# Kernel tuning notes

Measured on AMD Instinct MI355X. Metric: run time of the kernel, lower is better.

The kernel has to match this reference:

```python
import jax, jax.numpy as jnp
import numpy as np

N, E, G = 4096, 16384, 128   # nodes, edges, graphs
IN, H, ED = 64, 64, 16       # in_dim, hidden, edge_dim


def _lin(key, fan_in, fan_out):
    return jax.random.normal(key, (fan_in, fan_out), dtype=jnp.float32) * (fan_in ** -0.5)


def setup_inputs() -> dict:
    key = jax.random.key(0)
    ks = jax.random.split(key, 32)
    inp = {
        "x": jax.random.normal(ks[0], (N, IN), dtype=jnp.float32),
        "edge_index": jax.random.randint(ks[1], (2, E), 0, N, dtype=jnp.int32),
        "edge_attr": jax.random.normal(ks[2], (E, ED), dtype=jnp.float32),
        "batch": jnp.sort(jax.random.randint(ks[3], (N,), 0, G, dtype=jnp.int32)),
    }
    ki = 4
    dims = [(IN, H), (H, H), (H, H)]  # (in_channels, out_channels) per layer
    for l, (ic, oc) in enumerate(dims):
        hd = ic * oc  # edge-MLP width = hidden * in_channels
        inp[f"l{l}_w1"] = _lin(ks[ki], ED, hd); ki += 1
        inp[f"l{l}_b1"] = jnp.zeros((hd,), dtype=jnp.float32)
        inp[f"l{l}_w2"] = _lin(ks[ki], hd, hd); ki += 1
        inp[f"l{l}_b2"] = jnp.zeros((hd,), dtype=jnp.float32)
        inp[f"l{l}_root"] = _lin(ks[ki], ic, oc); ki += 1
        inp[f"l{l}_bias"] = jnp.zeros((oc,), dtype=jnp.float32)
    return inp


def _nnconv(x, src, dst, edge_attr, w1, b1, w2, b2, root, bias, ic, oc):
    # per-edge weight matrix Theta(e): [E, ic, oc]
    h = jax.nn.relu(edge_attr @ w1 + b1)
    theta = (h @ w2 + b2).reshape(-1, ic, oc)
    # gather source features, per-edge bmm, scatter-mean to target
    msg = jnp.einsum("ei,eio->eo", x[src], theta)
    agg = jax.ops.segment_sum(msg, dst, num_segments=N)
    cnt = jax.ops.segment_sum(jnp.ones((msg.shape[0],), msg.dtype), dst, num_segments=N)
    agg = agg / jnp.maximum(cnt, 1.0)[:, None]
    return agg + x @ root + bias


def reference(x, edge_index, edge_attr, batch,
              l0_w1, l0_b1, l0_w2, l0_b2, l0_root, l0_bias,
              l1_w1, l1_b1, l1_w2, l1_b2, l1_root, l1_bias,
              l2_w1, l2_b1, l2_w2, l2_b2, l2_root, l2_bias):
    src, dst = edge_index[0], edge_index[1]
    layers = [
        (l0_w1, l0_b1, l0_w2, l0_b2, l0_root, l0_bias, IN, H),
        (l1_w1, l1_b1, l1_w2, l1_b2, l1_root, l1_bias, H, H),
        (l2_w1, l2_b1, l2_w2, l2_b2, l2_root, l2_bias, H, H),
    ]
    h = x
    for (w1, b1, w2, b2, root, bias, ic, oc) in layers:
        h = jax.nn.relu(_nnconv(h, src, dst, edge_attr, w1, b1, w2, b2, root, bias, ic, oc))
        # dropout is identity in eval mode
    # global mean pool over graphs
    s = jax.ops.segment_sum(h, batch, num_segments=G)
    c = jax.ops.segment_sum(jnp.ones((N,), h.dtype), batch, num_segments=G)
    return s / jnp.maximum(c, 1.0)[:, None]
```

## Files before the change

### kernel.cpp

```cpp
#include <hip/hip_runtime.h>
#include <hip/hip_bf16.h>

#define NN 4096
#define EE 16384
#define GG 128
#define EDIM 16
#define HD 4096

#define NGROUPS 64
#define GK 8
#define KSUBS 64
#define MAXT 40
#define MAXSLOT (MAXT * 16)
#define MAXTW 5
#define SYUNITS (64 * 65 * 8)
#define PANEL (8 * 64 * 64)

typedef __attribute__((ext_vector_type(8))) short short8;
typedef __attribute__((ext_vector_type(4))) float float4v;

static __device__ inline unsigned short f2b(float f) {
    unsigned u = __float_as_uint(f);
    unsigned r = u + 0x7fff + ((u >> 16) & 1);
    return (unsigned short)(r >> 16);
}

static __device__ inline unsigned pk2(float a, float b) {
    __hip_bfloat162 p = __float22bfloat162_rn(make_float2(a, b));
    return *(unsigned*)&p;
}

__global__ void hker(const float* __restrict__ ea, const float* __restrict__ w1,
                     const float* __restrict__ b1, unsigned short* __restrict__ hB) {
    __shared__ float sea[16 * 16];
    const int tid = threadIdx.x;
    const int j = blockIdx.x * 256 + tid;
    const int e0 = blockIdx.y * 16;
    float w[16];
#pragma unroll
    for (int k = 0; k < 16; ++k) w[k] = w1[k * HD + j];
    const float b = b1[j];
    sea[tid] = ea[e0 * EDIM + tid];
    __syncthreads();
#pragma unroll 4
    for (int el = 0; el < 16; ++el) {
        float a = b;
#pragma unroll
        for (int k = 0; k < 16; ++k) a += sea[el * 16 + k] * w[k];
        hB[(size_t)(e0 + el) * HD + j] = f2b(fmaxf(a, 0.f));
    }
}

__global__ void wperm(const float* __restrict__ w2, unsigned short* __restrict__ W2q) {
    __shared__ float t[64 * 65];
    const int k = blockIdx.x;
    const int tid = threadIdx.x;
    const int o = tid & 63, r4 = tid >> 6;
#pragma unroll
    for (int it = 0; it < 16; ++it) {
        int i = it * 4 + r4;
        t[i * 65 + o] = w2[(size_t)k * HD + i * 64 + o];
    }
    __syncthreads();
    const int o2 = tid >> 2, q = tid & 3;
    const int q2 = q >> 1;
    const int j0 = (o2 >> 4) * 2 + q2;
    const int lmm = o2 & 15;
    const int blk = k;
#pragma unroll
    for (int cc = 0; cc < 2; ++cc) {
        const int quad = (q & 1) * 2 + cc;
        const int ib = q * 16 + cc * 8;
        size_t base = ((size_t)(blk * 64 + quad * 16 + lmm)) * 64 + j0 * 8;
        unsigned b0 = pk2(t[(ib + 0) * 65 + o2], t[(ib + 1) * 65 + o2]);
        unsigned b1 = pk2(t[(ib + 2) * 65 + o2], t[(ib + 3) * 65 + o2]);
        unsigned b2_ = pk2(t[(ib + 4) * 65 + o2], t[(ib + 5) * 65 + o2]);
        unsigned b3 = pk2(t[(ib + 6) * 65 + o2], t[(ib + 7) * 65 + o2]);
        *(uint4*)(&W2q[base]) = make_uint4(b0, b1, b2_, b3);
    }
}

__global__ void count_edges(const int* __restrict__ src, const int* __restrict__ dst,
                            int* __restrict__ cnt_src, float* __restrict__ cnt_dst) {
    const int e = blockIdx.x * 256 + threadIdx.x;
    atomicAdd(&cnt_src[src[e]], 1);
    atomicAdd(&cnt_dst[dst[e]], 1.f);
}

__global__ void build_layout(const int* __restrict__ cnt_src, int* __restrict__ node_slot_base,
                             int* __restrict__ tile_cluster, int* __restrict__ group_ntiles) {
    const int g = threadIdx.x;
    int nt = 0;
    int slot = g * MAXSLOT;
    for (int c = 0; c < 16; ++c) {
        int d = 0;
        for (int j = 0; j < 4; ++j) {
            int n = g * 64 + c * 4 + j;
            node_slot_base[n] = slot + d;
            d += cnt_src[n];
        }
        int tcnt = (d + 15) >> 4;
        if (nt + tcnt > MAXT) tcnt = MAXT - nt;
        for (int j = 0; j < tcnt; ++j) tile_cluster[g * MAXT + nt + j] = c;
        nt += tcnt;
        slot += tcnt * 16;
    }
    group_ntiles[g] = nt;
}

__global__ void fill_slots(const int* __restrict__ src, const int* __restrict__ dst,
                           int* __restrict__ fill, const int* __restrict__ node_slot_base,
                           int* __restrict__ slot_info) {
    const int e = blockIdx.x * 256 + threadIdx.x;
    const int n = src[e];
    const int pos = atomicAdd(&fill[n], 1);
    const int s = node_slot_base[n] + pos;
    const int g = n >> 6;
    if (s < g * MAXSLOT + MAXSLOT)
        slot_info[s] = e | ((n & 3) << 14) | (dst[e] << 16);
}

__global__ void xb_ker(const float* __restrict__ xcur, const float* __restrict__ b2,
                       float* __restrict__ xb) {
    const int n = blockIdx.x * 4 + (threadIdx.x >> 6);
    const int o = threadIdx.x & 63;
    float a = 0.f;
#pragma unroll
    for (int i = 0; i < 64; ++i) a += xcur[n * 64 + i] * b2[i * 64 + o];
    xb[n * 64 + o] = a;
}

__global__ void b2scatter(const float* __restrict__ xb, const int* __restrict__ src,
                          const int* __restrict__ dst, float* __restrict__ agg) {
    const int e = blockIdx.x * 4 + (threadIdx.x >> 6);
    const int o = threadIdx.x & 63;
    atomicAdd(&agg[(size_t)dst[e] * 64 + o], xb[(size_t)src[e] * 64 + o]);
}

__global__ __launch_bounds__(512, 2)
void ygemm_msg(const float* __restrict__ xcur, const unsigned short* __restrict__ hB,
               const unsigned short* __restrict__ W2q, const int* __restrict__ slot_info,
               const int* __restrict__ tile_cluster, const int* __restrict__ group_ntiles,
               float* __restrict__ agg) {
    __shared__ __align__(16) unsigned short sA[64 * 72];
    __shared__ __align__(16) unsigned short sY[2 * SYUNITS];

    const int bid = blockIdx.x;
    const int g = bid >> 3;
    const int kc = bid & 7;
    const int tid = threadIdx.x;
    const int lane = tid & 63, wave = tid >> 6;
    const int quad = lane >> 4, lm = lane & 15;

    {
        const int n = tid >> 3, ib = (tid & 7) * 8;
        const float* xp = xcur + (size_t)(g * 64 + n) * 64 + ib;
        uint4 w = make_uint4(pk2(xp[0], xp[1]), pk2(xp[2], xp[3]),
                             pk2(xp[4], xp[5]), pk2(xp[6], xp[7]));
        *(uint4*)(&sA[n * 72 + ib]) = w;
    }

    const int ntiles = group_ntiles[g];
    int infoR[MAXTW], voff[MAXTW], rbase[MAXTW];
    unsigned shl5[MAXTW];
#pragma unroll
    for (int ai = 0; ai < MAXTW; ++ai) {
        const int ti = wave + ai * 8;
        const int info = (ti < ntiles) ? slot_info[g * MAXSLOT + ti * 16 + lm] : -1;
        const int tc   = (ti < ntiles) ? tile_cluster[g * MAXT + ti] : 0;
        infoR[ai] = info;
        voff[ai]  = ((info >= 0) ? (info & 0x3FFF) : EE) * HD + quad * 2;
        rbase[ai] = ((tc * 4 + quad) * 65 + lm) * 8;
        shl5[ai]  = (unsigned)(((info >> 14) & 3) * 16);
    }

    float4v acc2[MAXTW][4];
#pragma unroll
    for (int a = 0; a < MAXTW; ++a)
#pragma unroll
        for (int t = 0; t < 4; ++t) {
            acc2[a][t][0] = 0.f; acc2[a][t][1] = 0.f;
            acc2[a][t][2] = 0.f; acc2[a][t][3] = 0.f;
        }

    const int qg = wave >> 1, half = wave & 1;
    const int wbase = ((quad * 4 + qg) * 65 + lm) * 8 + half * 4;
    __syncthreads();

    short8 af[4][2];
#pragma unroll
    for (int s = 0; s < 4; ++s)
#pragma unroll
        for (int q2 = 0; q2 < 2; ++q2)
            af[s][q2] = *(const short8*)(&sA[(s * 16 + lm) * 72 + q2 * 32 + quad * 8]);

    const float4v z4 = {0.f, 0.f, 0.f, 0.f};

    const unsigned short* wp  = W2q + ((size_t)(kc * KSUBS * 8 + wave) * 64 + lane) * 64;
    const unsigned short* hbk = hB + kc * KSUBS * 8;

    short8 bfA[4][2], bfB[4][2];
    unsigned hdA[MAXTW], hdB[MAXTW];
#pragma unroll
    for (int tt = 0; tt < 4; ++tt) {
        bfA[tt][0] = *(const short8*)(wp + (tt * 2 + 0) * 8);
        bfA[tt][1] = *(const short8*)(wp + (tt * 2 + 1) * 8);
    }
    wp += PANEL;
#pragma unroll
    for (int ai = 0; ai < MAXTW; ++ai) hdA[ai] = *(const unsigned*)(hbk + voff[ai]);
    hbk += 8;

    auto subody = [&](short8 (&BF)[4][2], unsigned (&HDc)[MAXTW],
                      short8 (&BFN)[4][2], unsigned (&HDN)[MAXTW],
                      unsigned short* __restrict__ sYp) {
#pragma unroll
        for (int s = 0; s < 4; ++s) {
            float4v a1[4];
#pragma unroll
            for (int tt = 0; tt < 4; ++tt)
                a1[tt] = __builtin_amdgcn_mfma_f32_16x16x32_bf16(af[s][0], BF[tt][0], z4, 0, 0, 0);
#pragma unroll
            for (int tt = 0; tt < 4; ++tt)
                a1[tt] = __builtin_amdgcn_mfma_f32_16x16x32_bf16(af[s][1], BF[tt][1], a1[tt], 0, 0, 0);
#pragma unroll
            for (int tt = 0; tt < 4; ++tt) {
                uint2 v;
                v.x = pk2(a1[tt][0], a1[tt][1]);
                v.y = pk2(a1[tt][2], a1[tt][3]);
                *(uint2*)(&sYp[wbase + s * 8320 + tt * 128]) = v;
            }
        }
        __syncthreads();

#pragma unroll
        for (int tt = 0; tt < 4; ++tt) {
            BFN[tt][0] = *(const short8*)(wp + (tt * 2 + 0) * 8);
            BFN[tt][1] = *(const short8*)(wp + (tt * 2 + 1) * 8);
        }
        wp += PANEL;
#pragma unroll
        for (int ai = 0; ai < MAXTW; ++ai)
            HDN[ai] = *(const unsigned*)(hbk + voff[ai]);
        hbk += 8;

#pragma unroll
        for (int ai = 0; ai < MAXTW; ++ai) {
            if (wave + ai * 8 < ntiles) {
                const unsigned h0 = HDc[ai];
                unsigned long long A = (unsigned long long)(h0 & 0xffffu) << shl5[ai];
                unsigned long long B = (unsigned long long)(h0 >> 16) << shl5[ai];
                uint4 aw = make_uint4((unsigned)A, (unsigned)(A >> 32),
                                      (unsigned)B, (unsigned)(B >> 32));
                short8 a2 = *(short8*)&aw;
#pragma unroll
                for (int ot = 0; ot < 4; ++ot) {
                    short8 b2f = *(const short8*)(&sYp[rbase[ai] + ot * 128]);
                    acc2[ai][ot] = __builtin_amdgcn_mfma_f32_16x16x32_bf16(a2, b2f, acc2[ai][ot], 0, 0, 0);
                }
            }
        }
    };

    for (int su2 = 0; su2 < KSUBS; su2 += 2) {
        subody(bfA, hdA, bfB, hdB, sY);
        subody(bfB, hdB, bfA, hdA, sY + SYUNITS);
    }

#pragma unroll
    for (int ai = 0; ai < MAXTW; ++ai) {
        const int ti = wave + ai * 8;
        if (ti < ntiles) {
#pragma unroll
            for (int r = 0; r < 4; ++r) {
                const int inf2 = __shfl(infoR[ai], quad * 4 + r, 64);
                if (inf2 >= 0) {
                    const int d = inf2 >> 16;
#pragma unroll
                    for (int ot = 0; ot < 4; ++ot)
                        atomicAdd(&agg[(size_t)d * 64 + ot * 16 + lm], acc2[ai][ot][r]);
                }
            }
        }
    }
}

__global__ void combine(const float* __restrict__ agg, const float* __restrict__ cnt,
                        const float* __restrict__ xcur, const float* __restrict__ root,
                        const float* __restrict__ bias, float* __restrict__ xn) {
    const int n = blockIdx.x * 4 + (threadIdx.x >> 6);
    const int o = threadIdx.x & 63;
    float a = agg[n * 64 + o] / fmaxf(cnt[n], 1.f);
    float r = bias[o];
#pragma unroll
    for (int i = 0; i < 64; ++i) r += xcur[n * 64 + i] * root[i * 64 + o];
    xn[n * 64 + o] = fmaxf(a + r, 0.f);
}

__global__ void pool_accum(const float* __restrict__ x3, const int* __restrict__ batch,
                           float* __restrict__ pool, float* __restrict__ pcnt) {
    const int n = blockIdx.x * 4 + (threadIdx.x >> 6);
    const int o = threadIdx.x & 63;
    const int gi = batch[n];
    atomicAdd(&pool[gi * 64 + o], x3[n * 64 + o]);
    if (o == 0) atomicAdd(&pcnt[gi], 1.f);
}

__global__ void pool_norm(const float* __restrict__ pool, const float* __restrict__ pcnt,
                          float* __restrict__ out) {
    const int idx = blockIdx.x * 256 + threadIdx.x;
    out[idx] = pool[idx] / fmaxf(pcnt[idx >> 6], 1.f);
}

extern "C" void kernel_launch(void* const* d_in, const int* in_sizes, int n_in,
                              void* d_out, int out_size, void* d_ws, size_t ws_size,
                              hipStream_t stream) {
    const float* x   = (const float*)d_in[0];
    const int*   ei  = (const int*)d_in[1];
    const float* ea  = (const float*)d_in[2];
    const int*   bat = (const int*)d_in[3];
    const int* srcp = ei;
    const int* dstp = ei + EE;

    char* ws = (char*)d_ws;
    size_t off = 0;
    unsigned short* hB  = (unsigned short*)(ws + off); off += (size_t)(EE + 1) * HD * 2;
    unsigned short* W2q = (unsigned short*)(ws + off); off += ((size_t)HD * HD + PANEL) * 2;
    int* slot_info      = (int*)(ws + off); off += (size_t)NGROUPS * MAXSLOT * 4;
    int* tile_cluster   = (int*)(ws + off); off += (size_t)NGROUPS * MAXT * 4;
    int* group_ntiles   = (int*)(ws + off); off += 1024;
    int* node_slot_base = (int*)(ws + off); off += (size_t)NN * 4;
    int* cnt_src        = (int*)(ws + off); off += (size_t)NN * 4;
    int* fillc          = (int*)(ws + off); off += (size_t)NN * 4;
    float* cnt_dst      = (float*)(ws + off); off += (size_t)NN * 4;
    float* agg  = (float*)(ws + off); off += (size_t)NN * 64 * 4;
    float* xb   = (float*)(ws + off); off += (size_t)NN * 64 * 4;
    float* xb0  = (float*)(ws + off); off += (size_t)NN * 64 * 4;
    float* xb1  = (float*)(ws + off); off += (size_t)NN * 64 * 4;
    float* pool = (float*)(ws + off); off += (size_t)GG * 64 * 4;
    float* pcnt = (float*)(ws + off); off += (size_t)GG * 4;

    hipMemsetAsync(slot_info, 0xFF, (size_t)NGROUPS * MAXSLOT * 4, stream);
    hipMemsetAsync(cnt_src, 0, (size_t)NN * 4 * 3, stream);
    hipMemsetAsync(hB + (size_t)EE * HD, 0, (size_t)HD * 2, stream);
    count_edges<<<EE / 256, 256, 0, stream>>>(srcp, dstp, cnt_src, cnt_dst);
    build_layout<<<1, 64, 0, stream>>>(cnt_src, node_slot_base, tile_cluster, group_ntiles);
    fill_slots<<<EE / 256, 256, 0, stream>>>(srcp, dstp, fillc, node_slot_base, slot_info);

    const float* xcur = x;
    float* xbufs[2] = {xb0, xb1};

    for (int l = 0; l < 3; ++l) {
        const float* w1   = (const float*)d_in[4 + 6 * l + 0];
        const float* b1   = (const float*)d_in[4 + 6 * l + 1];
        const float* w2   = (const float*)d_in[4 + 6 * l + 2];
        const float* b2   = (const float*)d_in[4 + 6 * l + 3];
        const float* root = (const float*)d_in[4 + 6 * l + 4];
        const float* bias = (const float*)d_in[4 + 6 * l + 5];

        wperm<<<HD, 256, 0, stream>>>(w2, W2q);
        hker<<<dim3(HD / 256, EE / 16), 256, 0, stream>>>(ea, w1, b1, hB);
        xb_ker<<<NN / 4, 256, 0, stream>>>(xcur, b2, xb);
        hipMemsetAsync(agg, 0, (size_t)NN * 64 * 4, stream);
        b2scatter<<<EE / 4, 256, 0, stream>>>(xb, srcp, dstp, agg);
        ygemm_msg<<<NGROUPS * GK, 512, 0, stream>>>(xcur, hB, W2q, slot_info,
                                                    tile_cluster, group_ntiles, agg);
        float* xn = xbufs[l & 1];
        combine<<<NN / 4, 256, 0, stream>>>(agg, cnt_dst, xcur, root, bias, xn);
        xcur = xn;
    }
    hipMemsetAsync(pool, 0, (size_t)GG * 64 * 4 + (size_t)GG * 4, stream);
    pool_accum<<<NN / 4, 256, 0, stream>>>(xcur, bat, pool, pcnt);
    pool_norm<<<GG * 64 / 256, 256, 0, stream>>>(pool, pcnt, (float*)d_out);
}
```

Baseline: 1.703 ms.

## Halve node groups to 32 nodes and use 256-thread blocks in message GEMM

Node groups shrink from 64 to 32 nodes, which doubles the number of groups and blocks, and each block drops to 4 waves. Each wave now covers its W2 panel in two k-halves per sub-step. The explicit double-buffered B-fragment prefetch is replaced by loading fragments inside the loop, with only the hB values prefetched one step ahead. The aim is more blocks across the CUs and lower per-block LDS and register pressure. The cost is that each W2 panel is now read by twice as many blocks, and the prefetch overlap for weight loads is lost.

Measured after the change: 2.076 ms. +21.9%, slower.

```diff
diff --git a/kernel.cpp b/kernel.cpp
--- a/kernel.cpp
+++ b/kernel.cpp
@@ -7,14 +7,15 @@
 #define EDIM 16
 #define HD 4096
 
-#define NGROUPS 64
+#define NGROUPS 128
 #define GK 8
 #define KSUBS 64
-#define MAXT 40
+#define MAXT 24
 #define MAXSLOT (MAXT * 16)
-#define MAXTW 5
-#define SYUNITS (64 * 65 * 8)
+#define MAXTW 6
+#define SYU 17152
 #define PANEL (8 * 64 * 64)
+#define KHOFF (4 * 64 * 64)
 
 typedef __attribute__((ext_vector_type(8))) short short8;
 typedef __attribute__((ext_vector_type(4))) float float4v;
@@ -92,10 +93,10 @@
     const int g = threadIdx.x;
     int nt = 0;
     int slot = g * MAXSLOT;
-    for (int c = 0; c < 16; ++c) {
+    for (int c = 0; c < 8; ++c) {
         int d = 0;
         for (int j = 0; j < 4; ++j) {
-            int n = g * 64 + c * 4 + j;
+            int n = g * 32 + c * 4 + j;
             node_slot_base[n] = slot + d;
             d += cnt_src[n];
         }
@@ -115,7 +116,7 @@
     const int n = src[e];
     const int pos = atomicAdd(&fill[n], 1);
     const int s = node_slot_base[n] + pos;
-    const int g = n >> 6;
+    const int g = n >> 5;
     if (s < g * MAXSLOT + MAXSLOT)
         slot_info[s] = e | ((n & 3) << 14) | (dst[e] << 16);
 }
@@ -137,13 +138,13 @@
     atomicAdd(&agg[(size_t)dst[e] * 64 + o], xb[(size_t)src[e] * 64 + o]);
 }
 
-__global__ __launch_bounds__(512, 2)
+__global__ __launch_bounds__(256, 2)
 void ygemm_msg(const float* __restrict__ xcur, const unsigned short* __restrict__ hB,
                const unsigned short* __restrict__ W2q, const int* __restrict__ slot_info,
                const int* __restrict__ tile_cluster, const int* __restrict__ group_ntiles,
                float* __restrict__ agg) {
-    __shared__ __align__(16) unsigned short sA[64 * 72];
-    __shared__ __align__(16) unsigned short sY[2 * SYUNITS];
+    __shared__ __align__(16) unsigned short sA[32 * 72];
+    __shared__ __align__(16) unsigned short sY[2 * SYU];
 
     const int bid = blockIdx.x;
     const int g = bid >> 3;
@@ -154,7 +155,7 @@
 
     {
         const int n = tid >> 3, ib = (tid & 7) * 8;
-        const float* xp = xcur + (size_t)(g * 64 + n) * 64 + ib;
+        const float* xp = xcur + (size_t)(g * 32 + n) * 64 + ib;
         uint4 w = make_uint4(pk2(xp[0], xp[1]), pk2(xp[2], xp[3]),
                              pk2(xp[4], xp[5]), pk2(xp[6], xp[7]));
         *(uint4*)(&sA[n * 72 + ib]) = w;
@@ -165,12 +166,12 @@
     unsigned shl5[MAXTW];
 #pragma unroll
     for (int ai = 0; ai < MAXTW; ++ai) {
-        const int ti = wave + ai * 8;
+        const int ti = wave + ai * 4;
         const int info = (ti < ntiles) ? slot_info[g * MAXSLOT + ti * 16 + lm] : -1;
         const int tc   = (ti < ntiles) ? tile_cluster[g * MAXT + ti] : 0;
         infoR[ai] = info;
         voff[ai]  = ((info >= 0) ? (info & 0x3FFF) : EE) * HD + quad * 2;
-        rbase[ai] = ((tc * 4 + quad) * 65 + lm) * 8;
+        rbase[ai] = ((tc * 4 + quad) * 67 + lm) * 8;
         shl5[ai]  = (unsigned)(((info >> 14) & 3) * 16);
     }
 
@@ -184,12 +185,12 @@
         }
 
     const int qg = wave >> 1, half = wave & 1;
-    const int wbase = ((quad * 4 + qg) * 65 + lm) * 8 + half * 4;
+    const int wb0 = ((quad * 4 + qg) * 67 + lm) * 8 + half * 4;
     __syncthreads();
 
-    short8 af[4][2];
-#pragma unroll
-    for (int s = 0; s < 4; ++s)
+    short8 af[2][2];
+#pragma unroll
+    for (int s = 0; s < 2; ++s)
 #pragma unroll
         for (int q2 = 0; q2 < 2; ++q2)
             af[s][q2] = *(const short8*)(&sA[(s * 16 + lm) * 72 + q2 * 32 + quad * 8]);
@@ -199,55 +200,54 @@
     const unsigned short* wp  = W2q + ((size_t)(kc * KSUBS * 8 + wave) * 64 + lane) * 64;
     const unsigned short* hbk = hB + kc * KSUBS * 8;
 
-    short8 bfA[4][2], bfB[4][2];
-    unsigned hdA[MAXTW], hdB[MAXTW];
-#pragma unroll
-    for (int tt = 0; tt < 4; ++tt) {
-        bfA[tt][0] = *(const short8*)(wp + (tt * 2 + 0) * 8);
-        bfA[tt][1] = *(const short8*)(wp + (tt * 2 + 1) * 8);
-    }
-    wp += PANEL;
-#pragma unroll
-    for (int ai = 0; ai < MAXTW; ++ai) hdA[ai] = *(const unsigned*)(hbk + voff[ai]);
-    hbk += 8;
-
-    auto subody = [&](short8 (&BF)[4][2], unsigned (&HDc)[MAXTW],
-                      short8 (&BFN)[4][2], unsigned (&HDN)[MAXTW],
-                      unsigned short* __restrict__ sYp) {
-#pragma unroll
-        for (int s = 0; s < 4; ++s) {
-            float4v a1[4];
-#pragma unroll
-            for (int tt = 0; tt < 4; ++tt)
-                a1[tt] = __builtin_amdgcn_mfma_f32_16x16x32_bf16(af[s][0], BF[tt][0], z4, 0, 0, 0);
-#pragma unroll
-            for (int tt = 0; tt < 4; ++tt)
-                a1[tt] = __builtin_amdgcn_mfma_f32_16x16x32_bf16(af[s][1], BF[tt][1], a1[tt], 0, 0, 0);
+    unsigned hd[MAXTW], hdN[MAXTW];
+#pragma unroll
+    for (int ai = 0; ai < MAXTW; ++ai) hd[ai] = *(const unsigned*)(hbk + voff[ai]);
+
+    for (int su = 0; su < KSUBS; ++su) {
+        unsigned short* sYp = sY + (su & 1) * SYU;
+
+#pragma unroll
+        for (int kh = 0; kh < 2; ++kh) {
+            short8 BF[4][2];
+            const unsigned short* wq = wp + kh * KHOFF;
 #pragma unroll
             for (int tt = 0; tt < 4; ++tt) {
-                uint2 v;
-                v.x = pk2(a1[tt][0], a1[tt][1]);
-                v.y = pk2(a1[tt][2], a1[tt][3]);
-                *(uint2*)(&sYp[wbase + s * 8320 + tt * 128]) = v;
+                BF[tt][0] = *(const short8*)(wq + (tt * 2 + 0) * 8);
+                BF[tt][1] = *(const short8*)(wq + (tt * 2 + 1) * 8);
             }
-        }
+            const int wb = wb0 + kh * 1072;
+#pragma unroll
+            for (int s = 0; s < 2; ++s) {
+                float4v a1[4];
+#pragma unroll
+                for (int tt = 0; tt < 4; ++tt)
+                    a1[tt] = __builtin_amdgcn_mfma_f32_16x16x32_bf16(af[s][0], BF[tt][0], z4, 0, 0, 0);
+#pragma unroll
+                for (int tt = 0; tt < 4; ++tt)
+                    a1[tt] = __builtin_amdgcn_mfma_f32_16x16x32_bf16(af[s][1], BF[tt][1], a1[tt], 0, 0, 0);
+#pragma unroll
+                for (int tt = 0; tt < 4; ++tt) {
+                    uint2 v;
+                    v.x = pk2(a1[tt][0], a1[tt][1]);
+                    v.y = pk2(a1[tt][2], a1[tt][3]);
+                    *(uint2*)(&sYp[wb + s * 8576 + tt * 128]) = v;
+                }
+            }
+        }
+        wp += PANEL;
+
+        const int sun = (su + 1 < KSUBS) ? su + 1 : su;
+#pragma unroll
+        for (int ai = 0; ai < MAXTW; ++ai)
+            hdN[ai] = *(const unsigned*)(hbk + sun * 8 + voff[ai]);
+
         __syncthreads();
 
 #pragma unroll
-        for (int tt = 0; tt < 4; ++tt) {
-            BFN[tt][0] = *(const short8*)(wp + (tt * 2 + 0) * 8);
-            BFN[tt][1] = *(const short8*)(wp + (tt * 2 + 1) * 8);
-        }
-        wp += PANEL;
-#pragma unroll
-        for (int ai = 0; ai < MAXTW; ++ai)
-            HDN[ai] = *(const unsigned*)(hbk + voff[ai]);
-        hbk += 8;
-
-#pragma unroll
         for (int ai = 0; ai < MAXTW; ++ai) {
-            if (wave + ai * 8 < ntiles) {
-                const unsigned h0 = HDc[ai];
+            if (wave + ai * 4 < ntiles) {
+                const unsigned h0 = hd[ai];
                 unsigned long long A = (unsigned long long)(h0 & 0xffffu) << shl5[ai];
                 unsigned long long B = (unsigned long long)(h0 >> 16) << shl5[ai];
                 uint4 aw = make_uint4((unsigned)A, (unsigned)(A >> 32),
@@ -260,16 +260,13 @@
                 }
             }
         }
-    };
-
-    for (int su2 = 0; su2 < KSUBS; su2 += 2) {
-        subody(bfA, hdA, bfB, hdB, sY);
-        subody(bfB, hdB, bfA, hdA, sY + SYUNITS);
+#pragma unroll
+        for (int ai = 0; ai < MAXTW; ++ai) hd[ai] = hdN[ai];
     }
 
 #pragma unroll
     for (int ai = 0; ai < MAXTW; ++ai) {
-        const int ti = wave + ai * 8;
+        const int ti = wave + ai * 4;
         if (ti < ntiles) {
 #pragma unroll
             for (int r = 0; r < 4; ++r) {
@@ -344,7 +341,7 @@
     hipMemsetAsync(cnt_src, 0, (size_t)NN * 4 * 3, stream);
     hipMemsetAsync(hB + (size_t)EE * HD, 0, (size_t)HD * 2, stream);
     count_edges<<<EE / 256, 256, 0, stream>>>(srcp, dstp, cnt_src, cnt_dst);
-    build_layout<<<1, 64, 0, stream>>>(cnt_src, node_slot_base, tile_cluster, group_ntiles);
+    build_layout<<<1, 128, 0, stream>>>(cnt_src, node_slot_base, tile_cluster, group_ntiles);
     fill_slots<<<EE / 256, 256, 0, stream>>>(srcp, dstp, fillc, node_slot_base, slot_info);
 
     const float* xcur = x;
@@ -363,7 +360,7 @@
         xb_ker<<<NN / 4, 256, 0, stream>>>(xcur, b2, xb);
         hipMemsetAsync(agg, 0, (size_t)NN * 64 * 4, stream);
         b2scatter<<<EE / 4, 256, 0, stream>>>(xb, srcp, dstp, agg);
-        ygemm_msg<<<NGROUPS * GK, 512, 0, stream>>>(xcur, hB, W2q, slot_info,
+        ygemm_msg<<<NGROUPS * GK, 256, 0, stream>>>(xcur, hB, W2q, slot_info,
                                                     tile_cluster, group_ntiles, agg);
         float* xn = xbufs[l & 1];
         combine<<<NN / 4, 256, 0, stream>>>(agg, cnt_dst, xcur, root, bias, xn);
```

## Swizzle sY LDS layout, single-buffer W2 fragments, prefetch hB two steps ahead

Applied to the files above, without the earlier changes.

Replaces the padded (stride 65) LDS layout for the intermediate Y tile with an XOR-swizzled 64-wide layout, reorganizing the offsets so the output-tile index is the outer stride. W2 fragments become a single register set reloaded after the barrier rather than double-buffered. hB values are now prefetched two sub-steps ahead, with clamped offsets. __syncthreads is replaced by an explicit lgkmcnt wait plus s_barrier. The aim is fewer LDS bank conflicts and lower register pressure, at the cost of less latency hiding for the W2 loads.

After: 1.621 ms. 4.8% less time.

```diff
diff --git a/kernel.cpp b/kernel.cpp
--- a/kernel.cpp
+++ b/kernel.cpp
@@ -13,7 +13,7 @@
 #define MAXT 40
 #define MAXSLOT (MAXT * 16)
 #define MAXTW 5
-#define SYUNITS (64 * 65 * 8)
+#define SYHALF (64 * 64 * 8)
 #define PANEL (8 * 64 * 64)
 
 typedef __attribute__((ext_vector_type(8))) short short8;
@@ -143,7 +143,7 @@
                const int* __restrict__ tile_cluster, const int* __restrict__ group_ntiles,
                float* __restrict__ agg) {
     __shared__ __align__(16) unsigned short sA[64 * 72];
-    __shared__ __align__(16) unsigned short sY[2 * SYUNITS];
+    __shared__ __align__(16) unsigned short sY[2 * SYHALF];
 
     const int bid = blockIdx.x;
     const int g = bid >> 3;
@@ -170,7 +170,7 @@
         const int tc   = (ti < ntiles) ? tile_cluster[g * MAXT + ti] : 0;
         infoR[ai] = info;
         voff[ai]  = ((info >= 0) ? (info & 0x3FFF) : EE) * HD + quad * 2;
-        rbase[ai] = ((tc * 4 + quad) * 65 + lm) * 8;
+        rbase[ai] = lm * 512 + (((tc * 4 + quad) ^ (lm & 7)) << 3);
         shl5[ai]  = (unsigned)(((info >> 14) & 3) * 16);
     }
 
@@ -184,7 +184,7 @@
         }
 
     const int qg = wave >> 1, half = wave & 1;
-    const int wbase = ((quad * 4 + qg) * 65 + lm) * 8 + half * 4;
+    const int wb = lm * 512 + (((quad * 4 + qg) ^ (lm & 7)) << 3) + half * 4;
     __syncthreads();
 
     short8 af[4][2];
@@ -199,21 +199,23 @@
     const unsigned short* wp  = W2q + ((size_t)(kc * KSUBS * 8 + wave) * 64 + lane) * 64;
     const unsigned short* hbk = hB + kc * KSUBS * 8;
 
-    short8 bfA[4][2], bfB[4][2];
+    short8 BF[4][2];
+#pragma unroll
+    for (int tt = 0; tt < 4; ++tt) {
+        BF[tt][0] = *(const short8*)(wp + (tt * 2 + 0) * 8);
+        BF[tt][1] = *(const short8*)(wp + (tt * 2 + 1) * 8);
+    }
+    wp += PANEL;
     unsigned hdA[MAXTW], hdB[MAXTW];
 #pragma unroll
-    for (int tt = 0; tt < 4; ++tt) {
-        bfA[tt][0] = *(const short8*)(wp + (tt * 2 + 0) * 8);
-        bfA[tt][1] = *(const short8*)(wp + (tt * 2 + 1) * 8);
-    }
-    wp += PANEL;
-#pragma unroll
-    for (int ai = 0; ai < MAXTW; ++ai) hdA[ai] = *(const unsigned*)(hbk + voff[ai]);
-    hbk += 8;
-
-    auto subody = [&](short8 (&BF)[4][2], unsigned (&HDc)[MAXTW],
-                      short8 (&BFN)[4][2], unsigned (&HDN)[MAXTW],
-                      unsigned short* __restrict__ sYp) {
+    for (int ai = 0; ai < MAXTW; ++ai) {
+        hdA[ai] = *(const unsigned*)(hbk + voff[ai]);
+        hdB[ai] = *(const unsigned*)(hbk + 8 + voff[ai]);
+    }
+
+    int hoff = 16;
+
+    auto subody = [&](unsigned (&HDc)[MAXTW], unsigned short* __restrict__ sYp) {
 #pragma unroll
         for (int s = 0; s < 4; ++s) {
             float4v a1[4];
@@ -228,21 +230,19 @@
                 uint2 v;
                 v.x = pk2(a1[tt][0], a1[tt][1]);
                 v.y = pk2(a1[tt][2], a1[tt][3]);
-                *(uint2*)(&sYp[wbase + s * 8320 + tt * 128]) = v;
+                *(uint2*)(&sYp[wb + s * 128 + tt * 8192]) = v;
             }
         }
-        __syncthreads();
+
+        asm volatile("s_waitcnt lgkmcnt(0)" ::: "memory");
+        __builtin_amdgcn_s_barrier();
 
 #pragma unroll
         for (int tt = 0; tt < 4; ++tt) {
-            BFN[tt][0] = *(const short8*)(wp + (tt * 2 + 0) * 8);
-            BFN[tt][1] = *(const short8*)(wp + (tt * 2 + 1) * 8);
+            BF[tt][0] = *(const short8*)(wp + (tt * 2 + 0) * 8);
+            BF[tt][1] = *(const short8*)(wp + (tt * 2 + 1) * 8);
         }
         wp += PANEL;
-#pragma unroll
-        for (int ai = 0; ai < MAXTW; ++ai)
-            HDN[ai] = *(const unsigned*)(hbk + voff[ai]);
-        hbk += 8;
 
 #pragma unroll
         for (int ai = 0; ai < MAXTW; ++ai) {
@@ -255,16 +255,21 @@
                 short8 a2 = *(short8*)&aw;
 #pragma unroll
                 for (int ot = 0; ot < 4; ++ot) {
-                    short8 b2f = *(const short8*)(&sYp[rbase[ai] + ot * 128]);
+                    short8 b2f = *(const short8*)(&sYp[rbase[ai] + ot * 8192]);
                     acc2[ai][ot] = __builtin_amdgcn_mfma_f32_16x16x32_bf16(a2, b2f, acc2[ai][ot], 0, 0, 0);
                 }
             }
         }
+
+#pragma unroll
+        for (int ai = 0; ai < MAXTW; ++ai)
+            HDc[ai] = *(const unsigned*)(hbk + hoff + voff[ai]);
+        hoff = (hoff < 504) ? hoff + 8 : 504;
     };
 
     for (int su2 = 0; su2 < KSUBS; su2 += 2) {
-        subody(bfA, hdA, bfB, hdB, sY);
-        subody(bfB, hdB, bfA, hdA, sY + SYUNITS);
+        subody(hdA, sY);
+        subody(hdB, sY + SYHALF);
     }
 
 #pragma unroll
```
